# Performance work log

Hardware: AMD Instinct MI355X
Metric: run time of the kernel (lower is better)

Reference implementation:

```python
import jax, jax.numpy as jnp
import numpy as np

ALPHA = 0.01  # matches LineFinderLoss(alpha=0.01)


def setup_inputs() -> dict:
    key = jax.random.key(0)
    k1, k2 = jax.random.split(key)
    S = 4096  # square so N == M == S (required for the original code to run)
    # column 4 is used as a probability: log(c) and log(1-c) must be finite
    inp = jax.random.uniform(k1, (S, S), dtype=jnp.float32, minval=1e-4, maxval=1.0 - 1e-4)
    tgt = jax.random.uniform(k2, (S, S), dtype=jnp.float32)
    return {"input": inp, "target": tgt}


def reference(input, target):
    N = input.shape[1]
    M = target.shape[1]
    # pairwise MSE cost over the first two coordinates: cost[n,m] = mean((input[n,:2]-target[m,:2])^2)
    diff = input[:, None, 0:2] - target[None, :, 0:2]  # [N, M, 2]
    cost = jnp.mean(diff * diff, axis=-1)              # [N, M]
    # Hungarian on an NxN cost yields a full assignment; the original code sets
    # X[p,l]=1 for the OUTER PRODUCT of matched row/col index sets, so X == ones
    # deterministically (matching does not affect the output).
    X = jnp.ones((N, M), dtype=input.dtype)
    mse_full = jnp.mean((input - target) ** 2)  # self.mse(input, target), constant over (n,m)
    log_c = jnpp_log = jnp.log(input[:, 4])     # [N]
    log_1mc = jnp.log(1.0 - input[:, 4])        # [N]
    # sum_{n,m} X*(alpha*mse_full - log c_n) - (1-X)*log(1-c_n)
    term = X * (ALPHA * mse_full - log_c[:, None]) - (1.0 - X) * log_1mc[:, None]
    # torch mse_loss(input[:,3], target) broadcasts (S,) against (S,S): elem [i,j] = (input[j,3]-target[i,j])^2
    loss = jnp.sum(term) + jnp.mean((input[:, 3] - target) ** 2)
    return loss, cost
```

## Files before the change

### kernel.cpp

```cpp
#include <hip/hip_runtime.h>

#define SDIM 4096
#define ALPHA 0.01f
#define WS_LOG 8
#define WS_ARR 128
#define WS_PART (WS_ARR + 5 * SDIM)
#define NRED 2048


__global__ void k_gather(const float* __restrict__ inp, const float* __restrict__ tgt,
                         float* __restrict__ ws) {
    int n = blockIdx.x * 64 + threadIdx.x;
    const float* row  = inp + (size_t)n * SDIM;
    const float* trow = tgt + (size_t)n * SDIM;
    float* arr = ws + WS_ARR;

    float v0 = row[0], v1 = row[1], v3 = row[3], v4 = row[4];
    arr[n]            = v0;
    arr[SDIM + n]     = v1;
    arr[2 * SDIM + n] = v3;
    int ns = (n + 1) & (SDIM - 1);
    arr[3 * SDIM + ns] = trow[0];
    arr[4 * SDIM + ns] = trow[1];

    float lg = logf(v4);
    #pragma unroll
    for (int off = 32; off > 0; off >>= 1) lg += __shfl_down(lg, off);
    if (threadIdx.x == 0) ws[WS_LOG + blockIdx.x] = lg;
}

__global__ void __launch_bounds__(256) k_fused(const float* __restrict__ inp,
                                               const float* __restrict__ tgt,
                                               const float* __restrict__ ws,
                                               float* __restrict__ out,
                                               float* __restrict__ wpart) {
    __shared__ float s1[4], s2[4];
    int bid = blockIdx.x;
    int t = threadIdx.x;
    const float* c0 = ws + WS_ARR;

    if (bid % 3 == 0) {
        int r = bid / 3;
        const float4* inp4 = (const float4*)inp;
        const float4* tgt4 = (const float4*)tgt;
        const float4* c34  = (const float4*)(c0 + 2 * SDIM);
        int base = r * 256 + t;
        float a1 = 0.f, a2 = 0.f, b1 = 0.f, b2 = 0.f;
        #pragma unroll
        for (int i = 0; i < 8; i += 2) {
            int ua = base + i * 524288;
            int ub = ua + 524288;
            float4 ia = inp4[ua], ta = tgt4[ua], ca = c34[ua & 1023];
            float4 ib = inp4[ub], tb = tgt4[ub], cb = c34[ub & 1023];
            float d;
            d = ia.x - ta.x; a1 += d * d;  d = ia.y - ta.y; a1 += d * d;
            d = ia.z - ta.z; a1 += d * d;  d = ia.w - ta.w; a1 += d * d;
            d = ca.x - ta.x; a2 += d * d;  d = ca.y - ta.y; a2 += d * d;
            d = ca.z - ta.z; a2 += d * d;  d = ca.w - ta.w; a2 += d * d;
            d = ib.x - tb.x; b1 += d * d;  d = ib.y - tb.y; b1 += d * d;
            d = ib.z - tb.z; b1 += d * d;  d = ib.w - tb.w; b1 += d * d;
            d = cb.x - tb.x; b2 += d * d;  d = cb.y - tb.y; b2 += d * d;
            d = cb.z - tb.z; b2 += d * d;  d = cb.w - tb.w; b2 += d * d;
        }
        a1 += b1; a2 += b2;
        #pragma unroll
        for (int off = 32; off > 0; off >>= 1) {
            a1 += __shfl_down(a1, off);
            a2 += __shfl_down(a2, off);
        }
        int wave = t >> 6;
        if ((t & 63) == 0) { s1[wave] = a1; s2[wave] = a2; }
        __syncthreads();
        if (t == 0) {
            wpart[r]        = s1[0] + s1[1] + s1[2] + s1[3];
            wpart[NRED + r] = s2[0] + s2[1] + s2[2] + s2[3];
        }
    } else {
        int n = 2 * (bid / 3) + (bid % 3) - 1;
        const float* c1 = c0 + SDIM;
        const float4* u04 = (const float4*)(c0 + 3 * SDIM);
        const float4* u14 = (const float4*)(c0 + 4 * SDIM);
        float a0 = c0[n], b0 = c1[n];
        float4* orow4 = (float4*)(out + (size_t)n * SDIM);
        #pragma unroll
        for (int k = 0; k < 4; ++k) {
            int j = k * 256 + t;
            float4 U0 = u04[j], U1 = u14[j];
            float e0, e1;
            float4 v;
            e0 = a0 - U0.x; e1 = b0 - U1.x; v.x = 0.5f * (e0 * e0 + e1 * e1);
            e0 = a0 - U0.y; e1 = b0 - U1.y; v.y = 0.5f * (e0 * e0 + e1 * e1);
            e0 = a0 - U0.z; e1 = b0 - U1.z; v.z = 0.5f * (e0 * e0 + e1 * e1);
            e0 = a0 - U0.w; e1 = b0 - U1.w; v.w = 0.5f * (e0 * e0 + e1 * e1);
            if (j == 0) {
                if (n == 0) {
                    v.x = 0.0f;
                } else {
                    float ap = c0[n - 1], bp = c1[n - 1];
                    e0 = ap - U0.x; e1 = bp - U1.x;
                    v.x = 0.5f * (e0 * e0 + e1 * e1);
                }
            }
            orow4[j] = v;
        }
        if (n == SDIM - 1 && t == 255) {
            const float* u0 = c0 + 3 * SDIM;
            const float* u1 = c0 + 4 * SDIM;
            float e0 = a0 - u0[0], e1 = b0 - u1[0];
            out[(size_t)SDIM * SDIM] = 0.5f * (e0 * e0 + e1 * e1);
        }
    }
}

__global__ void k_final(const float* __restrict__ ws, float* __restrict__ out) {
    __shared__ float s1[4], s2[4];
    float a1 = 0.0f, a2 = 0.0f;
    const float* wpart = ws + WS_PART;
    for (int i = threadIdx.x; i < NRED; i += 256) {
        a1 += wpart[i];
        a2 += wpart[NRED + i];
    }
    #pragma unroll
    for (int off = 32; off > 0; off >>= 1) {
        a1 += __shfl_down(a1, off);
        a2 += __shfl_down(a2, off);
    }
    int wave = threadIdx.x >> 6;
    if ((threadIdx.x & 63) == 0) { s1[wave] = a1; s2[wave] = a2; }
    __syncthreads();
    if (threadIdx.x == 0) {
        float sum_sq = s1[0] + s1[1] + s1[2] + s1[3];
        float sum3   = s2[0] + s2[1] + s2[2] + s2[3];
        float slog = 0.0f;
        #pragma unroll
        for (int i = 0; i < 64; ++i) slog += ws[WS_LOG + i];
        out[0] = ALPHA * sum_sq - (float)SDIM * slog
               + sum3 * (1.0f / ((float)SDIM * (float)SDIM));
    }
}

extern "C" void kernel_launch(void* const* d_in, const int* in_sizes, int n_in,
                              void* d_out, int out_size, void* d_ws, size_t ws_size,
                              hipStream_t stream) {
    const float* inp = (const float*)d_in[0];
    const float* tgt = (const float*)d_in[1];
    float* out = (float*)d_out;
    float* ws  = (float*)d_ws;

    k_gather<<<64, 64, 0, stream>>>(inp, tgt, ws);
    k_fused<<<6144, 256, 0, stream>>>(inp, tgt, ws, out, ws + WS_PART);
    k_final<<<1, 256, 0, stream>>>(ws, out);
}
```

Before: 185.4 us.

## Split fused kernel into separate write and reduce kernels with nontemporal stores

Replaces the interleaved fused kernel, whose block roles alternated between reduction and output writing, with two separate kernels: one writes two cost rows per block using nontemporal stores, the other performs the MSE reductions. The write kernel loads the target columns once and reuses them for both rows. The reduce kernel hoists the per-thread constant column load out of the loop, since the index stays the same across chunks. This adds a kernel launch and removes the overlap between the write-bound and read-bound phases.

```diff
diff --git a/kernel.cpp b/kernel.cpp
--- a/kernel.cpp
+++ b/kernel.cpp
@@ -6,6 +6,9 @@
 #define WS_ARR 128
 #define WS_PART (WS_ARR + 5 * SDIM)
 #define NRED 2048
+#define CHUNK 524288
+
+using nfloat4 = __attribute__((ext_vector_type(4))) float;
 
 
 __global__ void k_gather(const float* __restrict__ inp, const float* __restrict__ tgt,
@@ -29,86 +32,106 @@
     if (threadIdx.x == 0) ws[WS_LOG + blockIdx.x] = lg;
 }
 
-__global__ void __launch_bounds__(256) k_fused(const float* __restrict__ inp,
-                                               const float* __restrict__ tgt,
-                                               const float* __restrict__ ws,
-                                               float* __restrict__ out,
-                                               float* __restrict__ wpart) {
+__global__ void __launch_bounds__(256) k_write(const float* __restrict__ ws,
+                                               float* __restrict__ out) {
+    int b = blockIdx.x;
+    int t = threadIdx.x;
+    int n0 = 2 * b, n1 = 2 * b + 1;
+    const float* c0 = ws + WS_ARR;
+    const float* c1 = c0 + SDIM;
+    const float4* u04 = (const float4*)(c0 + 3 * SDIM);
+    const float4* u14 = (const float4*)(c0 + 4 * SDIM);
+
+    float a00 = c0[n0], b00 = c1[n0];
+    float a01 = c0[n1], b01 = c1[n1];
+
+    float4 U0[4], U1[4];
+    #pragma unroll
+    for (int k = 0; k < 4; ++k) {
+        U0[k] = u04[k * 256 + t];
+        U1[k] = u14[k * 256 + t];
+    }
+
+    nfloat4* orow0 = (nfloat4*)(out + (size_t)n0 * SDIM);
+    nfloat4* orow1 = (nfloat4*)(out + (size_t)n1 * SDIM);
+    #pragma unroll
+    for (int k = 0; k < 4; ++k) {
+        int j = k * 256 + t;
+        float e0, e1;
+        nfloat4 v0, v1;
+        e0 = a00 - U0[k].x; e1 = b00 - U1[k].x; v0.x = 0.5f * (e0 * e0 + e1 * e1);
+        e0 = a00 - U0[k].y; e1 = b00 - U1[k].y; v0.y = 0.5f * (e0 * e0 + e1 * e1);
+        e0 = a00 - U0[k].z; e1 = b00 - U1[k].z; v0.z = 0.5f * (e0 * e0 + e1 * e1);
+        e0 = a00 - U0[k].w; e1 = b00 - U1[k].w; v0.w = 0.5f * (e0 * e0 + e1 * e1);
+        e0 = a01 - U0[k].x; e1 = b01 - U1[k].x; v1.x = 0.5f * (e0 * e0 + e1 * e1);
+        e0 = a01 - U0[k].y; e1 = b01 - U1[k].y; v1.y = 0.5f * (e0 * e0 + e1 * e1);
+        e0 = a01 - U0[k].z; e1 = b01 - U1[k].z; v1.z = 0.5f * (e0 * e0 + e1 * e1);
+        e0 = a01 - U0[k].w; e1 = b01 - U1[k].w; v1.w = 0.5f * (e0 * e0 + e1 * e1);
+        if (j == 0) {
+            if (n0 == 0) {
+                v0.x = 0.0f;
+            } else {
+                float ap = c0[n0 - 1], bp = c1[n0 - 1];
+                e0 = ap - U0[0].x; e1 = bp - U1[0].x;
+                v0.x = 0.5f * (e0 * e0 + e1 * e1);
+            }
+            e0 = a00 - U0[0].x; e1 = b00 - U1[0].x;
+            v1.x = 0.5f * (e0 * e0 + e1 * e1);
+        }
+        __builtin_nontemporal_store(v0, &orow0[j]);
+        __builtin_nontemporal_store(v1, &orow1[j]);
+    }
+    if (n1 == SDIM - 1 && t == 255) {
+        const float* u0 = c0 + 3 * SDIM;
+        const float* u1 = c0 + 4 * SDIM;
+        float e0 = a01 - u0[0], e1 = b01 - u1[0];
+        out[(size_t)SDIM * SDIM] = 0.5f * (e0 * e0 + e1 * e1);
+    }
+}
+
+__global__ void __launch_bounds__(256) k_reduce(const float* __restrict__ inp,
+                                                const float* __restrict__ tgt,
+                                                const float* __restrict__ ws,
+                                                float* __restrict__ wpart) {
     __shared__ float s1[4], s2[4];
-    int bid = blockIdx.x;
+    int r = blockIdx.x;
     int t = threadIdx.x;
     const float* c0 = ws + WS_ARR;
+    const float4* inp4 = (const float4*)inp;
+    const float4* tgt4 = (const float4*)tgt;
+    const float4* c34  = (const float4*)(c0 + 2 * SDIM);
+    int base = r * 256 + t;
+    float4 ca = c34[base & 1023];
+    float a1 = 0.f, a2 = 0.f, b1 = 0.f, b2 = 0.f;
 
-    if (bid % 3 == 0) {
-        int r = bid / 3;
-        const float4* inp4 = (const float4*)inp;
-        const float4* tgt4 = (const float4*)tgt;
-        const float4* c34  = (const float4*)(c0 + 2 * SDIM);
-        int base = r * 256 + t;
-        float a1 = 0.f, a2 = 0.f, b1 = 0.f, b2 = 0.f;
-        #pragma unroll
-        for (int i = 0; i < 8; i += 2) {
-            int ua = base + i * 524288;
-            int ub = ua + 524288;
-            float4 ia = inp4[ua], ta = tgt4[ua], ca = c34[ua & 1023];
-            float4 ib = inp4[ub], tb = tgt4[ub], cb = c34[ub & 1023];
-            float d;
-            d = ia.x - ta.x; a1 += d * d;  d = ia.y - ta.y; a1 += d * d;
-            d = ia.z - ta.z; a1 += d * d;  d = ia.w - ta.w; a1 += d * d;
-            d = ca.x - ta.x; a2 += d * d;  d = ca.y - ta.y; a2 += d * d;
-            d = ca.z - ta.z; a2 += d * d;  d = ca.w - ta.w; a2 += d * d;
-            d = ib.x - tb.x; b1 += d * d;  d = ib.y - tb.y; b1 += d * d;
-            d = ib.z - tb.z; b1 += d * d;  d = ib.w - tb.w; b1 += d * d;
-            d = cb.x - tb.x; b2 += d * d;  d = cb.y - tb.y; b2 += d * d;
-            d = cb.z - tb.z; b2 += d * d;  d = cb.w - tb.w; b2 += d * d;
-        }
-        a1 += b1; a2 += b2;
-        #pragma unroll
-        for (int off = 32; off > 0; off >>= 1) {
-            a1 += __shfl_down(a1, off);
-            a2 += __shfl_down(a2, off);
-        }
-        int wave = t >> 6;
-        if ((t & 63) == 0) { s1[wave] = a1; s2[wave] = a2; }
-        __syncthreads();
-        if (t == 0) {
-            wpart[r]        = s1[0] + s1[1] + s1[2] + s1[3];
-            wpart[NRED + r] = s2[0] + s2[1] + s2[2] + s2[3];
-        }
-    } else {
-        int n = 2 * (bid / 3) + (bid % 3) - 1;
-        const float* c1 = c0 + SDIM;
-        const float4* u04 = (const float4*)(c0 + 3 * SDIM);
-        const float4* u14 = (const float4*)(c0 + 4 * SDIM);
-        float a0 = c0[n], b0 = c1[n];
-        float4* orow4 = (float4*)(out + (size_t)n * SDIM);
-        #pragma unroll
-        for (int k = 0; k < 4; ++k) {
-            int j = k * 256 + t;
-            float4 U0 = u04[j], U1 = u14[j];
-            float e0, e1;
-            float4 v;
-            e0 = a0 - U0.x; e1 = b0 - U1.x; v.x = 0.5f * (e0 * e0 + e1 * e1);
-            e0 = a0 - U0.y; e1 = b0 - U1.y; v.y = 0.5f * (e0 * e0 + e1 * e1);
-            e0 = a0 - U0.z; e1 = b0 - U1.z; v.z = 0.5f * (e0 * e0 + e1 * e1);
-            e0 = a0 - U0.w; e1 = b0 - U1.w; v.w = 0.5f * (e0 * e0 + e1 * e1);
-            if (j == 0) {
-                if (n == 0) {
-                    v.x = 0.0f;
-                } else {
-                    float ap = c0[n - 1], bp = c1[n - 1];
-                    e0 = ap - U0.x; e1 = bp - U1.x;
-                    v.x = 0.5f * (e0 * e0 + e1 * e1);
-                }
-            }
-            orow4[j] = v;
-        }
-        if (n == SDIM - 1 && t == 255) {
-            const float* u0 = c0 + 3 * SDIM;
-            const float* u1 = c0 + 4 * SDIM;
-            float e0 = a0 - u0[0], e1 = b0 - u1[0];
-            out[(size_t)SDIM * SDIM] = 0.5f * (e0 * e0 + e1 * e1);
-        }
+    #pragma unroll
+    for (int g = 0; g < 8; g += 2) {
+        int ua = base + g * CHUNK;
+        int ub = ua + CHUNK;
+        float4 ia = inp4[ua], ta = tgt4[ua];
+        float4 ib = inp4[ub], tb = tgt4[ub];
+        float d;
+        d = ia.x - ta.x; a1 += d * d;  d = ia.y - ta.y; a1 += d * d;
+        d = ia.z - ta.z; a1 += d * d;  d = ia.w - ta.w; a1 += d * d;
+        d = ca.x - ta.x; a2 += d * d;  d = ca.y - ta.y; a2 += d * d;
+        d = ca.z - ta.z; a2 += d * d;  d = ca.w - ta.w; a2 += d * d;
+        d = ib.x - tb.x; b1 += d * d;  d = ib.y - tb.y; b1 += d * d;
+        d = ib.z - tb.z; b1 += d * d;  d = ib.w - tb.w; b1 += d * d;
+        d = ca.x - tb.x; b2 += d * d;  d = ca.y - tb.y; b2 += d * d;
+        d = ca.z - tb.z; b2 += d * d;  d = ca.w - tb.w; b2 += d * d;
+    }
+    a1 += b1; a2 += b2;
+    #pragma unroll
+    for (int off = 32; off > 0; off >>= 1) {
+        a1 += __shfl_down(a1, off);
+        a2 += __shfl_down(a2, off);
+    }
+    int wave = t >> 6;
+    if ((t & 63) == 0) { s1[wave] = a1; s2[wave] = a2; }
+    __syncthreads();
+    if (t == 0) {
+        wpart[r]        = s1[0] + s1[1] + s1[2] + s1[3];
+        wpart[NRED + r] = s2[0] + s2[1] + s2[2] + s2[3];
     }
 }
 
@@ -148,6 +171,7 @@
     float* ws  = (float*)d_ws;
 
     k_gather<<<64, 64, 0, stream>>>(inp, tgt, ws);
-    k_fused<<<6144, 256, 0, stream>>>(inp, tgt, ws, out, ws + WS_PART);
+    k_write<<<NRED, 256, 0, stream>>>(ws, out);
+    k_reduce<<<NRED, 256, 0, stream>>>(inp, tgt, ws, ws + WS_PART);
     k_final<<<1, 256, 0, stream>>>(ws, out);
 }
```

After: 177.5 us. -4.2%, faster.
